# Performance work log

Hardware: AMD Instinct MI355X
Metric: run time of the kernel (lower is better)

Reference implementation:

```python
import jax, jax.numpy as jnp
import numpy as np

B, H, W, C = 1, 64, 64, 256
HEADS, K, DIL = 8, 7, 2
HD = C // HEADS
FF = 4 * C
EPS = 1e-5
SCALE = 1.0 / float(np.sqrt(HD))


def _axis_indices(L, k, d):
    """NATTEN dilated neighborhood: per dilation-group clamped sliding window.
    Returns key indices [L,k] and relative-position-bias indices [L,k]."""
    i = np.arange(L)
    g, rem = i // d, i % d                      # position within dilation group
    lg = (L - rem + d - 1) // d                 # group length per position
    start = np.clip(g - k // 2, 0, lg - k)      # clamped window start (group coords)
    a = np.arange(k)
    kidx = (start[:, None] + a[None, :]) * d + rem[:, None]          # key coord
    bidx = start[:, None] + a[None, :] - g[:, None] + (k - 1)        # rpb coord in [0, 2k-2]
    return kidx.astype(np.int32), bidx.astype(np.int32)


def setup_inputs():
    key = jax.random.key(0)
    ks = jax.random.split(key, 8)
    p = lambda k_, sh: jax.random.normal(k_, sh, jnp.float32) * 0.02
    return {
        "x": jax.random.normal(ks[0], (B, H, W, C), jnp.float32),
        "ln1_g": jnp.ones((C,), jnp.float32), "ln1_b": jnp.zeros((C,), jnp.float32),
        "wq": p(ks[1], (C, C)), "bq": jnp.zeros((C,), jnp.float32),
        "wk": p(ks[2], (C, C)), "bk": jnp.zeros((C,), jnp.float32),
        "wv": p(ks[3], (C, C)), "bv": jnp.zeros((C,), jnp.float32),
        "rpb": p(ks[4], (HEADS, 2 * K - 1, 2 * K - 1)),
        "wo": p(ks[5], (C, C)), "bo": jnp.zeros((C,), jnp.float32),
        "ln2_g": jnp.ones((C,), jnp.float32), "ln2_b": jnp.zeros((C,), jnp.float32),
        "w1": p(ks[6], (C, FF)), "b1": jnp.zeros((FF,), jnp.float32),
        "w2": p(ks[7], (FF, C)), "b2": jnp.zeros((C,), jnp.float32),
    }


def _layer_norm(x, g, b):
    m = jnp.mean(x, -1, keepdims=True)
    v = jnp.mean(jnp.square(x - m), -1, keepdims=True)
    return (x - m) * jax.lax.rsqrt(v + EPS) * g + b


def reference(x, ln1_g, ln1_b, wq, bq, wk, bk, wv, bv, rpb, wo, bo,
              ln2_g, ln2_b, w1, b1, w2, b2):
    ih, bih = _axis_indices(H, K, DIL)   # [H,K]
    iw, biw = _axis_indices(W, K, DIL)   # [W,K]
    hs = _layer_norm(x, ln1_g, ln1_b)
    q = (hs @ wq + bq).reshape(B, H, W, HEADS, HD) * SCALE
    k = (hs @ wk + bk).reshape(B, H, W, HEADS, HD)
    v = (hs @ wv + bv).reshape(B, H, W, HEADS, HD)
    # gather dilated neighborhoods -> [B,H,W,K,K,heads,hd]
    k_nb = k[:, ih[:, None, :, None], iw[None, :, None, :], :, :]
    v_nb = v[:, ih[:, None, :, None], iw[None, :, None, :], :, :]
    # natten2dqkrpb: per-query scores over K*K dilated neighbors + rpb
    scores = jnp.einsum('bijnc,bijklnc->bnijkl', q, k_nb)
    bias = rpb[:, bih[:, None, :, None], biw[None, :, None, :]]  # [heads,H,W,K,K]
    scores = scores + bias[None]
    probs = jax.nn.softmax(scores.reshape(B, HEADS, H, W, K * K), axis=-1)
    # natten2dav
    ctx = jnp.einsum('bnijp,bijpnc->bijnc', probs,
                     v_nb.reshape(B, H, W, K * K, HEADS, HD))
    attn_out = ctx.reshape(B, H, W, C) @ wo + bo
    hs2 = x + attn_out                      # residual (layer_scale disabled: init 0.0)
    y = _layer_norm(hs2, ln2_g, ln2_b)
    y = jax.nn.gelu(y @ w1 + b1, approximate=False) @ w2 + b2
    return hs2 + y
```

## Files before the change

kernel.cpp:

```cpp
#include <hip/hip_runtime.h>
#include <math.h>

#define CC 256
#define NTOK 4096
#define NHEADS 8
#define HD 32
#define FFD 1024
#define LN_EPS 1e-5f
#define QSCALE 0.17677669529663687f

typedef __bf16 bf16x8 __attribute__((ext_vector_type(8)));
typedef float f32x4 __attribute__((ext_vector_type(4)));
typedef unsigned short u16x8 __attribute__((ext_vector_type(8)));

__device__ __forceinline__ unsigned short f2bf(float f) {
    unsigned u = __builtin_bit_cast(unsigned, f);
    u += 0x7fff + ((u >> 16) & 1);
    return (unsigned short)(u >> 16);
}
__device__ __forceinline__ float bf2f(unsigned short h) {
    unsigned u = ((unsigned)h) << 16;
    return __builtin_bit_cast(float, u);
}
__device__ __forceinline__ void gload16(const unsigned short* g, unsigned short* l) {
    __builtin_amdgcn_global_load_lds(
        (const __attribute__((address_space(1))) unsigned int*)(const void*)g,
        (__attribute__((address_space(3))) unsigned int*)(void*)l, 16, 0, 0);
}

__device__ __forceinline__ void ln_row(const float* __restrict__ x, const float* __restrict__ g,
                                       const float* __restrict__ b, unsigned short* __restrict__ out,
                                       int tok, int lane) {
    const float4 v = ((const float4*)(x + (size_t)tok * CC))[lane];
    float s  = v.x + v.y + v.z + v.w;
    float ss = v.x * v.x + v.y * v.y + v.z * v.z + v.w * v.w;
    #pragma unroll
    for (int o = 32; o > 0; o >>= 1) { s += __shfl_xor(s, o); ss += __shfl_xor(ss, o); }
    float m   = s * (1.0f / CC);
    float var = ss * (1.0f / CC) - m * m;
    float r   = rsqrtf(var + LN_EPS);
    float4 gv = ((const float4*)g)[lane];
    float4 bv = ((const float4*)b)[lane];
    ushort4 o4;
    o4.x = f2bf((v.x - m) * r * gv.x + bv.x);
    o4.y = f2bf((v.y - m) * r * gv.y + bv.y);
    o4.z = f2bf((v.z - m) * r * gv.z + bv.z);
    o4.w = f2bf((v.w - m) * r * gv.w + bv.w);
    ((ushort4*)(out + (size_t)tok * CC))[lane] = o4;
}

__global__ void ln_kernel(const float* __restrict__ x, const float* __restrict__ g,
                          const float* __restrict__ b, unsigned short* __restrict__ out) {
    ln_row(x, g, b, out, blockIdx.x * 4 + (threadIdx.x >> 6), threadIdx.x & 63);
}

__global__ void setup_kernel(const float* __restrict__ wq, const float* __restrict__ wk,
                             const float* __restrict__ wv, const float* __restrict__ wo,
                             const float* __restrict__ w1, const float* __restrict__ w2,
                             const float* __restrict__ bq, const float* __restrict__ bk,
                             const float* __restrict__ bv,
                             const float* __restrict__ x, const float* __restrict__ ln1_g,
                             const float* __restrict__ ln1_b,
                             unsigned short* __restrict__ wt_qkv, unsigned short* __restrict__ wo_t,
                             unsigned short* __restrict__ w1_t, unsigned short* __restrict__ w2_t,
                             float* __restrict__ bqkv, unsigned short* __restrict__ hs_bf) {
    int id = blockIdx.x;
    int t = threadIdx.x;
    if (id >= 193) {
        ln_row(x, ln1_g, ln1_b, hs_bf, (id - 193) * 4 + (t >> 6), t & 63);
        return;
    }
    if (id == 192) {
        bqkv[t]       = bq[t] * QSCALE;
        bqkv[256 + t] = bk[t];
        bqkv[512 + t] = bv[t];
        return;
    }
    const float* src; unsigned short* dst;
    int Kd, N, rowoff = 0, bx, by; float scale = 1.0f;
    if (id < 16)       { src = wq; dst = wt_qkv; Kd = 256;  N = 256;  scale = QSCALE; int l = id;       bx = l & 3;  by = l >> 2; }
    else if (id < 32)  { src = wk; dst = wt_qkv; Kd = 256;  N = 256;  rowoff = 256;   int l = id - 16;  bx = l & 3;  by = l >> 2; }
    else if (id < 48)  { src = wv; dst = wt_qkv; Kd = 256;  N = 256;  rowoff = 512;   int l = id - 32;  bx = l & 3;  by = l >> 2; }
    else if (id < 64)  { src = wo; dst = wo_t;   Kd = 256;  N = 256;                  int l = id - 48;  bx = l & 3;  by = l >> 2; }
    else if (id < 128) { src = w1; dst = w1_t;   Kd = 256;  N = 1024;                 int l = id - 64;  bx = l & 15; by = l >> 4; }
    else               { src = w2; dst = w2_t;   Kd = 1024; N = 256;                  int l = id - 128; bx = l & 3;  by = l >> 2; }
    int n0 = bx * 64, k0 = by * 64;
    __shared__ float tile[64][65];
    int cc = t & 63, rb = t >> 6;
    #pragma unroll
    for (int i = 0; i < 16; i++) {
        int r = rb + i * 4;
        tile[r][cc] = src[(size_t)(k0 + r) * N + n0 + cc];
    }
    __syncthreads();
    int n = t >> 2;
    #pragma unroll
    for (int i = 0; i < 8; i++) {
        int p = (t & 3) + i * 4;
        unsigned lo = f2bf(tile[2 * p][n] * scale);
        unsigned hi = f2bf(tile[2 * p + 1][n] * scale);
        *(unsigned*)(dst + (size_t)(rowoff + n0 + n) * Kd + k0 + 2 * p) = lo | (hi << 16);
    }
}

template<int BM, int BN, int KD, int ACT, bool ADD_RES, bool OUT_BF16>
__global__ __launch_bounds__(256) void gemm_tb(
    const unsigned short* __restrict__ A, const unsigned short* __restrict__ Bt,
    const float* __restrict__ bias, const float* __restrict__ res,
    void* __restrict__ Cm, int N) {
    constexpr int WM = BM / 2, WN = BN / 2;
    constexpr int MF = WM / 16, NF = WN / 16;
    constexpr int NIT = KD / 64;
    constexpr int LA = BM * 8 / 256;
    constexpr int LB = BN * 8 / 256;
    constexpr int L  = LA + LB;
    __shared__ unsigned short lds[3][(BM + BN) * 64];
    const int t = threadIdx.x;
    const int lane = t & 63, w = t >> 6;
    const int wr = w >> 1, wc = w & 1;
    const int bm = blockIdx.y * BM, bn = blockIdx.x * BN;
    const int fr = lane & 15, sq = lane >> 4;

    auto stage = [&](int it, int buf) {
        unsigned short* La = lds[buf];
        unsigned short* Lb = lds[buf] + BM * 64;
        #pragma unroll
        for (int i = 0; i < LA; i++) {
            int c = t + i * 256;
            int kk = c / (BM * 4), r = (c % (BM * 4)) >> 2, jj = c & 3;
            gload16(A + (size_t)(bm + r) * KD + it * 64 + kk * 32 + jj * 8, La + c * 8);
        }
        #pragma unroll
        for (int i = 0; i < LB; i++) {
            int c = t + i * 256;
            int kk = c / (BN * 4), r = (c % (BN * 4)) >> 2, jj = c & 3;
            gload16(Bt + (size_t)(bn + r) * KD + it * 64 + kk * 32 + jj * 8, Lb + c * 8);
        }
    };

    f32x4 acc[MF][NF] = {};
    stage(0, 0);
    stage(1, 1);
    #pragma unroll
    for (int it = 0; it < NIT; ++it) {
        if (it < NIT - 1) {
            if constexpr (L == 4) asm volatile("s_waitcnt vmcnt(4)" ::: "memory");
            else if constexpr (L == 3) asm volatile("s_waitcnt vmcnt(3)" ::: "memory");
            else asm volatile("s_waitcnt vmcnt(2)" ::: "memory");
        } else {
            asm volatile("s_waitcnt vmcnt(0)" ::: "memory");
        }
        __builtin_amdgcn_s_barrier();
        if (it + 2 < NIT) stage(it + 2, (it + 2) % 3);
        const int buf = it % 3;
        #pragma unroll
        for (int kk = 0; kk < 2; kk++) {
            const char* La = (const char*)(lds[buf]) + kk * BM * 64;
            const char* Lb = (const char*)(lds[buf] + BM * 64) + kk * BN * 64;
            bf16x8 af[MF], bfr[NF];
            #pragma unroll
            for (int i = 0; i < MF; i++)
                af[i] = *(const bf16x8*)(La + (wr * WM + i * 16 + fr) * 64 + sq * 16);
            #pragma unroll
            for (int j = 0; j < NF; j++)
                bfr[j] = *(const bf16x8*)(Lb + (wc * WN + j * 16 + fr) * 64 + sq * 16);
            #pragma unroll
            for (int i = 0; i < MF; i++)
                #pragma unroll
                for (int j = 0; j < NF; j++)
                    acc[i][j] = __builtin_amdgcn_mfma_f32_16x16x32_bf16(af[i], bfr[j], acc[i][j], 0, 0, 0);
        }
    }
    #pragma unroll
    for (int i = 0; i < MF; i++) {
        int row0 = bm + wr * WM + i * 16 + sq * 4;
        #pragma unroll
        for (int j = 0; j < NF; j++) {
            int col = bn + wc * WN + j * 16 + fr;
            float bvv = bias[col];
            #pragma unroll
            for (int r = 0; r < 4; r++) {
                float v = acc[i][j][r] + bvv;
                if constexpr (ACT == 1) v = 0.5f * v * (1.0f + erff(v * 0.70710678118654752f));
                if constexpr (ADD_RES) v += res[(size_t)(row0 + r) * N + col];
                if constexpr (OUT_BF16)
                    ((unsigned short*)Cm)[(size_t)(row0 + r) * N + col] = f2bf(v);
                else
                    ((float*)Cm)[(size_t)(row0 + r) * N + col] = v;
            }
        }
    }
}

__global__ __launch_bounds__(256) void attn_mfma(
    const unsigned short* __restrict__ qkv, const float* __restrict__ rpb,
    unsigned short* __restrict__ ctx) {
    __shared__ __align__(16) unsigned short VT[128][136];
    __shared__ __align__(16) unsigned short Pl[4][16][136];
    __shared__ unsigned short tbl[16][112];
    __shared__ float rpbl[4][172];

    const int t = threadIdx.x;
    const int lane = t & 63, w = t >> 6;
    const int fr = lane & 15, sq = lane >> 4;
    const int bid = blockIdx.x;
    const int p = bid & 3, tile = (bid >> 2) & 63, hb = bid >> 8;
    const int ri = p >> 1, rj = p & 1;
    const int tgi = (tile >> 3) * 4, tgj = (tile & 7) * 4;
    const int kgi0 = min(max(tgi - 3, 0), 22);
    const int kgj0 = min(max(tgj - 3, 0), 22);
    const int head = hb * 4 + w;

    for (int i = lane; i < 169; i += 64)
        rpbl[w][i] = rpb[head * 169 + i];
    if (lane == 0) rpbl[w][169] = -1e30f;

    for (int e = t; e < 16 * 112; e += 256) {
        int q = e / 112, kk = e % 112;
        unsigned short idx = 169;
        if (kk < 100) {
            int kr = kk / 10, kc = kk % 10;
            int qgi = tgi + (q >> 2), qgj = tgj + (q & 3);
            int kgi = kgi0 + kr, kgj = kgj0 + kc;
            int si = min(max(qgi - 3, 0), 25), sj = min(max(qgj - 3, 0), 25);
            if (kgi >= si && kgi <= si + 6 && kgj >= sj && kgj <= sj + 6)
                idx = (unsigned short)((kgi - qgi + 6) * 13 + (kgj - qgj + 6));
        }
        tbl[q][kk] = idx;
    }

    for (int c0 = t; c0 < 1600; c0 += 256) {
        int key = c0 >> 4, ch8 = c0 & 15;
        int kr = key / 10, kc = key % 10;
        int kt = ((kgi0 + kr) * 2 + ri) * 64 + (kgj0 + kc) * 2 + rj;
        u16x8 vv = *(const u16x8*)(qkv + (size_t)kt * 768 + 512 + hb * 128 + ch8 * 8);
        #pragma unroll
        for (int e = 0; e < 8; e++) VT[ch8 * 8 + e][key] = vv[e];
    }
    for (int c0 = t; c0 < 128 * 14; c0 += 256) {
        int row = c0 / 14, cp = c0 % 14;
        *(unsigned*)&VT[row][100 + cp * 2] = 0;
    }
    __syncthreads();

    const int qtok = ((tgi + (fr >> 2)) * 2 + ri) * 64 + (tgj + (fr & 3)) * 2 + rj;
    bf16x8 qf = *(const bf16x8*)(qkv + (size_t)qtok * 768 + head * 32 + sq * 8);

    f32x4 sc[7];
    __builtin_amdgcn_s_setprio(1);
    #pragma unroll
    for (int c = 0; c < 7; c++) {
        int kk = c * 16 + fr;
        if (kk > 99) kk = 99;
        int kr = kk / 10, kc = kk % 10;
        int kt = ((kgi0 + kr) * 2 + ri) * 64 + (kgj0 + kc) * 2 + rj;
        bf16x8 kf = *(const bf16x8*)(qkv + (size_t)kt * 768 + 256 + head * 32 + sq * 8);
        f32x4 z = {0.0f, 0.0f, 0.0f, 0.0f};
        sc[c] = __builtin_amdgcn_mfma_f32_16x16x32_bf16(kf, qf, z, 0, 0, 0);
    }
    __builtin_amdgcn_s_setprio(0);
    #pragma unroll
    for (int c = 0; c < 7; c++)
        #pragma unroll
        for (int r = 0; r < 4; r++) {
            int idx = tbl[fr][c * 16 + 4 * sq + r];
            sc[c][r] += rpbl[w][idx];
        }

    float mx = -1e30f;
    #pragma unroll
    for (int c = 0; c < 7; c++)
        #pragma unroll
        for (int r = 0; r < 4; r++) mx = fmaxf(mx, sc[c][r]);
    mx = fmaxf(mx, __shfl_xor(mx, 16));
    mx = fmaxf(mx, __shfl_xor(mx, 32));
    float sum = 0.0f;
    #pragma unroll
    for (int c = 0; c < 7; c++)
        #pragma unroll
        for (int r = 0; r < 4; r++) {
            sc[c][r] = __expf(sc[c][r] - mx);
            sum += sc[c][r];
        }
    sum += __shfl_xor(sum, 16);
    sum += __shfl_xor(sum, 32);
    float inv = 1.0f / sum;

    #pragma unroll
    for (int c = 0; c < 7; c++)
        #pragma unroll
        for (int r = 0; r < 4; r++)
            Pl[w][fr][c * 16 + 4 * sq + r] = f2bf(sc[c][r] * inv);
    *(unsigned long long*)&Pl[w][fr][112 + sq * 4] = 0ull;

    f32x4 o0 = {0, 0, 0, 0}, o1 = {0, 0, 0, 0};
    __builtin_amdgcn_s_setprio(1);
    #pragma unroll
    for (int m = 0; m < 4; m++) {
        bf16x8 pf = *(const bf16x8*)(&Pl[w][fr][m * 32 + sq * 8]);
        bf16x8 v0 = *(const bf16x8*)(&VT[w * 32 + fr][m * 32 + sq * 8]);
        bf16x8 v1 = *(const bf16x8*)(&VT[w * 32 + 16 + fr][m * 32 + sq * 8]);
        o0 = __builtin_amdgcn_mfma_f32_16x16x32_bf16(pf, v0, o0, 0, 0, 0);
        o1 = __builtin_amdgcn_mfma_f32_16x16x32_bf16(pf, v1, o1, 0, 0, 0);
    }
    __builtin_amdgcn_s_setprio(0);
    #pragma unroll
    for (int r = 0; r < 4; r++) {
        int tok = ((tgi + sq) * 2 + ri) * 64 + (tgj + r) * 2 + rj;
        ctx[(size_t)tok * 256 + head * 32 + fr]      = f2bf(o0[r]);
        ctx[(size_t)tok * 256 + head * 32 + 16 + fr] = f2bf(o1[r]);
    }
}

extern "C" void kernel_launch(void* const* d_in, const int* in_sizes, int n_in,
                              void* d_out, int out_size, void* d_ws, size_t ws_size,
                              hipStream_t stream) {
    const float* x     = (const float*)d_in[0];
    const float* ln1_g = (const float*)d_in[1];
    const float* ln1_b = (const float*)d_in[2];
    const float* wq    = (const float*)d_in[3];
    const float* bq    = (const float*)d_in[4];
    const float* wk    = (const float*)d_in[5];
    const float* bk    = (const float*)d_in[6];
    const float* wv    = (const float*)d_in[7];
    const float* bv    = (const float*)d_in[8];
    const float* rpb   = (const float*)d_in[9];
    const float* wo    = (const float*)d_in[10];
    const float* bo    = (const float*)d_in[11];
    const float* ln2_g = (const float*)d_in[12];
    const float* ln2_b = (const float*)d_in[13];
    const float* w1    = (const float*)d_in[14];
    const float* b1    = (const float*)d_in[15];
    const float* w2    = (const float*)d_in[16];
    const float* b2    = (const float*)d_in[17];

    char* wsb = (char*)d_ws;
    unsigned short* hs_bf  = (unsigned short*)(wsb);
    unsigned short* qkv_bf = (unsigned short*)(wsb + (2u << 20));
    unsigned short* ctx_bf = (unsigned short*)(wsb + (8u << 20));
    float*          hs2    = (float*)(wsb + (10u << 20));
    unsigned short* y1_bf  = (unsigned short*)(wsb + (14u << 20));
    unsigned short* gm_bf  = (unsigned short*)(wsb + (16u << 20));
    unsigned short* wt_qkv = (unsigned short*)(wsb + (24u << 20));
    unsigned short* wo_t   = wt_qkv + 768 * 256;
    unsigned short* w1_t   = wo_t + 256 * 256;
    unsigned short* w2_t   = w1_t + 1024 * 256;
    float*          bqkv   = (float*)(w2_t + 256 * 1024);

    setup_kernel<<<1217, 256, 0, stream>>>(wq, wk, wv, wo, w1, w2, bq, bk, bv,
                                           x, ln1_g, ln1_b,
                                           wt_qkv, wo_t, w1_t, w2_t, bqkv, hs_bf);
    gemm_tb<64, 64, 256, 0, false, true><<<dim3(12, 64), 256, 0, stream>>>(
        hs_bf, wt_qkv, bqkv, nullptr, qkv_bf, 768);
    attn_mfma<<<512, 256, 0, stream>>>(qkv_bf, rpb, ctx_bf);
    gemm_tb<32, 64, 256, 0, true, false><<<dim3(4, 128), 256, 0, stream>>>(
        ctx_bf, wo_t, bo, x, hs2, 256);
    ln_kernel<<<NTOK / 4, 256, 0, stream>>>(hs2, ln2_g, ln2_b, y1_bf);
    gemm_tb<64, 64, 256, 1, false, true><<<dim3(16, 64), 256, 0, stream>>>(
        y1_bf, w1_t, b1, nullptr, gm_bf, 1024);
    gemm_tb<32, 64, 1024, 0, true, false><<<dim3(4, 128), 256, 0, stream>>>(
        gm_bf, w2_t, b2, hs2, (float*)d_out, 256);
}
```

Baseline: 133.8 us.

## Fuse all stages into one persistent kernel with atomic grid barriers

Replaces seven separate kernel launches with a single persistent kernel of 256 blocks. Each block loops over its share of tiles for every stage, and stages are separated by a software grid barrier built on an atomic counter and sleep polling. The aim is to remove launch overhead and inter-kernel gaps. In exchange, 256 blocks may underfill the GPU for the GEMM and attention stages, the spin barrier adds its own cost, and correctness depends on all blocks being co-resident.

Result: slower. 246.1 us (+83.9%).

```diff
diff --git a/kernel.cpp b/kernel.cpp
--- a/kernel.cpp
+++ b/kernel.cpp
@@ -3,11 +3,9 @@
 
 #define CC 256
 #define NTOK 4096
-#define NHEADS 8
-#define HD 32
-#define FFD 1024
 #define LN_EPS 1e-5f
 #define QSCALE 0.17677669529663687f
+#define NBLK 256
 
 typedef __bf16 bf16x8 __attribute__((ext_vector_type(8)));
 typedef float f32x4 __attribute__((ext_vector_type(4)));
@@ -26,6 +24,18 @@
     __builtin_amdgcn_global_load_lds(
         (const __attribute__((address_space(1))) unsigned int*)(const void*)g,
         (__attribute__((address_space(3))) unsigned int*)(void*)l, 16, 0, 0);
+}
+
+__device__ __forceinline__ void grid_sync(unsigned* bar) {
+    __syncthreads();
+    if (threadIdx.x == 0) {
+        __threadfence();
+        unsigned old = atomicAdd(bar, 1u);
+        unsigned target = (old / NBLK + 1u) * NBLK;
+        while (atomicAdd(bar, 0u) < target) __builtin_amdgcn_s_sleep(8);
+        __threadfence();
+    }
+    __syncthreads();
 }
 
 __device__ __forceinline__ void ln_row(const float* __restrict__ x, const float* __restrict__ g,
@@ -49,81 +59,27 @@
     ((ushort4*)(out + (size_t)tok * CC))[lane] = o4;
 }
 
-__global__ void ln_kernel(const float* __restrict__ x, const float* __restrict__ g,
-                          const float* __restrict__ b, unsigned short* __restrict__ out) {
-    ln_row(x, g, b, out, blockIdx.x * 4 + (threadIdx.x >> 6), threadIdx.x & 63);
-}
-
-__global__ void setup_kernel(const float* __restrict__ wq, const float* __restrict__ wk,
-                             const float* __restrict__ wv, const float* __restrict__ wo,
-                             const float* __restrict__ w1, const float* __restrict__ w2,
-                             const float* __restrict__ bq, const float* __restrict__ bk,
-                             const float* __restrict__ bv,
-                             const float* __restrict__ x, const float* __restrict__ ln1_g,
-                             const float* __restrict__ ln1_b,
-                             unsigned short* __restrict__ wt_qkv, unsigned short* __restrict__ wo_t,
-                             unsigned short* __restrict__ w1_t, unsigned short* __restrict__ w2_t,
-                             float* __restrict__ bqkv, unsigned short* __restrict__ hs_bf) {
-    int id = blockIdx.x;
-    int t = threadIdx.x;
-    if (id >= 193) {
-        ln_row(x, ln1_g, ln1_b, hs_bf, (id - 193) * 4 + (t >> 6), t & 63);
-        return;
-    }
-    if (id == 192) {
-        bqkv[t]       = bq[t] * QSCALE;
-        bqkv[256 + t] = bk[t];
-        bqkv[512 + t] = bv[t];
-        return;
-    }
-    const float* src; unsigned short* dst;
-    int Kd, N, rowoff = 0, bx, by; float scale = 1.0f;
-    if (id < 16)       { src = wq; dst = wt_qkv; Kd = 256;  N = 256;  scale = QSCALE; int l = id;       bx = l & 3;  by = l >> 2; }
-    else if (id < 32)  { src = wk; dst = wt_qkv; Kd = 256;  N = 256;  rowoff = 256;   int l = id - 16;  bx = l & 3;  by = l >> 2; }
-    else if (id < 48)  { src = wv; dst = wt_qkv; Kd = 256;  N = 256;  rowoff = 512;   int l = id - 32;  bx = l & 3;  by = l >> 2; }
-    else if (id < 64)  { src = wo; dst = wo_t;   Kd = 256;  N = 256;                  int l = id - 48;  bx = l & 3;  by = l >> 2; }
-    else if (id < 128) { src = w1; dst = w1_t;   Kd = 256;  N = 1024;                 int l = id - 64;  bx = l & 15; by = l >> 4; }
-    else               { src = w2; dst = w2_t;   Kd = 1024; N = 256;                  int l = id - 128; bx = l & 3;  by = l >> 2; }
-    int n0 = bx * 64, k0 = by * 64;
-    __shared__ float tile[64][65];
-    int cc = t & 63, rb = t >> 6;
-    #pragma unroll
-    for (int i = 0; i < 16; i++) {
-        int r = rb + i * 4;
-        tile[r][cc] = src[(size_t)(k0 + r) * N + n0 + cc];
-    }
-    __syncthreads();
-    int n = t >> 2;
-    #pragma unroll
-    for (int i = 0; i < 8; i++) {
-        int p = (t & 3) + i * 4;
-        unsigned lo = f2bf(tile[2 * p][n] * scale);
-        unsigned hi = f2bf(tile[2 * p + 1][n] * scale);
-        *(unsigned*)(dst + (size_t)(rowoff + n0 + n) * Kd + k0 + 2 * p) = lo | (hi << 16);
-    }
-}
-
 template<int BM, int BN, int KD, int ACT, bool ADD_RES, bool OUT_BF16>
-__global__ __launch_bounds__(256) void gemm_tb(
-    const unsigned short* __restrict__ A, const unsigned short* __restrict__ Bt,
-    const float* __restrict__ bias, const float* __restrict__ res,
-    void* __restrict__ Cm, int N) {
+__device__ void gemm_tile(char* smem, const unsigned short* __restrict__ A,
+                          const unsigned short* __restrict__ Bt,
+                          const float* __restrict__ bias, const float* __restrict__ res,
+                          void* __restrict__ Cm, int N, int bm, int bn) {
     constexpr int WM = BM / 2, WN = BN / 2;
     constexpr int MF = WM / 16, NF = WN / 16;
     constexpr int NIT = KD / 64;
     constexpr int LA = BM * 8 / 256;
     constexpr int LB = BN * 8 / 256;
     constexpr int L  = LA + LB;
-    __shared__ unsigned short lds[3][(BM + BN) * 64];
+    constexpr int BUFE = (BM + BN) * 64;
+    unsigned short* lds = (unsigned short*)smem;
     const int t = threadIdx.x;
     const int lane = t & 63, w = t >> 6;
     const int wr = w >> 1, wc = w & 1;
-    const int bm = blockIdx.y * BM, bn = blockIdx.x * BN;
     const int fr = lane & 15, sq = lane >> 4;
 
     auto stage = [&](int it, int buf) {
-        unsigned short* La = lds[buf];
-        unsigned short* Lb = lds[buf] + BM * 64;
+        unsigned short* La = lds + buf * BUFE;
+        unsigned short* Lb = La + BM * 64;
         #pragma unroll
         for (int i = 0; i < LA; i++) {
             int c = t + i * 256;
@@ -141,22 +97,20 @@
     f32x4 acc[MF][NF] = {};
     stage(0, 0);
     stage(1, 1);
-    #pragma unroll
     for (int it = 0; it < NIT; ++it) {
         if (it < NIT - 1) {
             if constexpr (L == 4) asm volatile("s_waitcnt vmcnt(4)" ::: "memory");
-            else if constexpr (L == 3) asm volatile("s_waitcnt vmcnt(3)" ::: "memory");
-            else asm volatile("s_waitcnt vmcnt(2)" ::: "memory");
+            else asm volatile("s_waitcnt vmcnt(3)" ::: "memory");
         } else {
             asm volatile("s_waitcnt vmcnt(0)" ::: "memory");
         }
         __builtin_amdgcn_s_barrier();
         if (it + 2 < NIT) stage(it + 2, (it + 2) % 3);
-        const int buf = it % 3;
+        const char* Lab = (const char*)(lds + (it % 3) * BUFE);
         #pragma unroll
         for (int kk = 0; kk < 2; kk++) {
-            const char* La = (const char*)(lds[buf]) + kk * BM * 64;
-            const char* Lb = (const char*)(lds[buf] + BM * 64) + kk * BN * 64;
+            const char* La = Lab + kk * BM * 64;
+            const char* Lb = Lab + BM * 128 + kk * BN * 64;
             bf16x8 af[MF], bfr[NF];
             #pragma unroll
             for (int i = 0; i < MF; i++)
@@ -190,30 +144,33 @@
             }
         }
     }
-}
-
-__global__ __launch_bounds__(256) void attn_mfma(
-    const unsigned short* __restrict__ qkv, const float* __restrict__ rpb,
-    unsigned short* __restrict__ ctx) {
-    __shared__ __align__(16) unsigned short VT[128][136];
-    __shared__ __align__(16) unsigned short Pl[4][16][136];
-    __shared__ unsigned short tbl[16][112];
-    __shared__ float rpbl[4][172];
+    asm volatile("s_waitcnt vmcnt(0)" ::: "memory");
+    __syncthreads();
+}
+
+__device__ void attn_unit(char* smem, const unsigned short* __restrict__ qkv,
+                          const float* __restrict__ rpb, unsigned short* __restrict__ ctx,
+                          int unit) {
+    unsigned short* VT  = (unsigned short*)smem;
+    unsigned short* Pl  = VT + 128 * 136;
+    unsigned short* tbl = Pl + 4 * 16 * 136;
+    float*          rpbl = (float*)(tbl + 16 * 112);
 
     const int t = threadIdx.x;
     const int lane = t & 63, w = t >> 6;
     const int fr = lane & 15, sq = lane >> 4;
-    const int bid = blockIdx.x;
-    const int p = bid & 3, tile = (bid >> 2) & 63, hb = bid >> 8;
+    const int p = unit & 3, tile = (unit >> 2) & 63, hb = unit >> 8;
     const int ri = p >> 1, rj = p & 1;
     const int tgi = (tile >> 3) * 4, tgj = (tile & 7) * 4;
     const int kgi0 = min(max(tgi - 3, 0), 22);
     const int kgj0 = min(max(tgj - 3, 0), 22);
     const int head = hb * 4 + w;
 
+    __syncthreads();
+
     for (int i = lane; i < 169; i += 64)
-        rpbl[w][i] = rpb[head * 169 + i];
-    if (lane == 0) rpbl[w][169] = -1e30f;
+        rpbl[w * 172 + i] = rpb[head * 169 + i];
+    if (lane == 0) rpbl[w * 172 + 169] = -1e30f;
 
     for (int e = t; e < 16 * 112; e += 256) {
         int q = e / 112, kk = e % 112;
@@ -226,7 +183,7 @@
             if (kgi >= si && kgi <= si + 6 && kgj >= sj && kgj <= sj + 6)
                 idx = (unsigned short)((kgi - qgi + 6) * 13 + (kgj - qgj + 6));
         }
-        tbl[q][kk] = idx;
+        tbl[q * 112 + kk] = idx;
     }
 
     for (int c0 = t; c0 < 1600; c0 += 256) {
@@ -235,11 +192,11 @@
         int kt = ((kgi0 + kr) * 2 + ri) * 64 + (kgj0 + kc) * 2 + rj;
         u16x8 vv = *(const u16x8*)(qkv + (size_t)kt * 768 + 512 + hb * 128 + ch8 * 8);
         #pragma unroll
-        for (int e = 0; e < 8; e++) VT[ch8 * 8 + e][key] = vv[e];
+        for (int e = 0; e < 8; e++) VT[(ch8 * 8 + e) * 136 + key] = vv[e];
     }
     for (int c0 = t; c0 < 128 * 14; c0 += 256) {
         int row = c0 / 14, cp = c0 % 14;
-        *(unsigned*)&VT[row][100 + cp * 2] = 0;
+        *(unsigned*)&VT[row * 136 + 100 + cp * 2] = 0;
     }
     __syncthreads();
 
@@ -262,10 +219,8 @@
     #pragma unroll
     for (int c = 0; c < 7; c++)
         #pragma unroll
-        for (int r = 0; r < 4; r++) {
-            int idx = tbl[fr][c * 16 + 4 * sq + r];
-            sc[c][r] += rpbl[w][idx];
-        }
+        for (int r = 0; r < 4; r++)
+            sc[c][r] += rpbl[w * 172 + tbl[fr * 112 + c * 16 + 4 * sq + r]];
 
     float mx = -1e30f;
     #pragma unroll
@@ -290,16 +245,16 @@
     for (int c = 0; c < 7; c++)
         #pragma unroll
         for (int r = 0; r < 4; r++)
-            Pl[w][fr][c * 16 + 4 * sq + r] = f2bf(sc[c][r] * inv);
-    *(unsigned long long*)&Pl[w][fr][112 + sq * 4] = 0ull;
+            Pl[(w * 16 + fr) * 136 + c * 16 + 4 * sq + r] = f2bf(sc[c][r] * inv);
+    *(unsigned long long*)&Pl[(w * 16 + fr) * 136 + 112 + sq * 4] = 0ull;
 
     f32x4 o0 = {0, 0, 0, 0}, o1 = {0, 0, 0, 0};
     __builtin_amdgcn_s_setprio(1);
     #pragma unroll
     for (int m = 0; m < 4; m++) {
-        bf16x8 pf = *(const bf16x8*)(&Pl[w][fr][m * 32 + sq * 8]);
-        bf16x8 v0 = *(const bf16x8*)(&VT[w * 32 + fr][m * 32 + sq * 8]);
-        bf16x8 v1 = *(const bf16x8*)(&VT[w * 32 + 16 + fr][m * 32 + sq * 8]);
+        bf16x8 pf = *(const bf16x8*)(&Pl[(w * 16 + fr) * 136 + m * 32 + sq * 8]);
+        bf16x8 v0 = *(const bf16x8*)(&VT[(w * 32 + fr) * 136 + m * 32 + sq * 8]);
+        bf16x8 v1 = *(const bf16x8*)(&VT[(w * 32 + 16 + fr) * 136 + m * 32 + sq * 8]);
         o0 = __builtin_amdgcn_mfma_f32_16x16x32_bf16(pf, v0, o0, 0, 0, 0);
         o1 = __builtin_amdgcn_mfma_f32_16x16x32_bf16(pf, v1, o1, 0, 0, 0);
     }
@@ -309,6 +264,104 @@
         int tok = ((tgi + sq) * 2 + ri) * 64 + (tgj + r) * 2 + rj;
         ctx[(size_t)tok * 256 + head * 32 + fr]      = f2bf(o0[r]);
         ctx[(size_t)tok * 256 + head * 32 + 16 + fr] = f2bf(o1[r]);
+    }
+}
+
+__global__ __launch_bounds__(256) void mega(
+    const float* __restrict__ x,
+    const float* __restrict__ ln1_g, const float* __restrict__ ln1_b,
+    const float* __restrict__ wq, const float* __restrict__ bq,
+    const float* __restrict__ wk, const float* __restrict__ bk,
+    const float* __restrict__ wv, const float* __restrict__ bv,
+    const float* __restrict__ rpb,
+    const float* __restrict__ wo, const float* __restrict__ bo,
+    const float* __restrict__ ln2_g, const float* __restrict__ ln2_b,
+    const float* __restrict__ w1, const float* __restrict__ b1,
+    const float* __restrict__ w2, const float* __restrict__ b2,
+    unsigned short* __restrict__ hs_bf, unsigned short* __restrict__ qkv_bf,
+    unsigned short* __restrict__ ctx_bf, float* __restrict__ hs2,
+    unsigned short* __restrict__ y1_bf, unsigned short* __restrict__ gm_bf,
+    unsigned short* __restrict__ wt_qkv, unsigned short* __restrict__ wo_t,
+    unsigned short* __restrict__ w1_t, unsigned short* __restrict__ w2_t,
+    float* __restrict__ bqkv, float* __restrict__ out, unsigned* bar) {
+    __shared__ __align__(16) char smem[58560];
+    const int b = blockIdx.x;
+    const int t = threadIdx.x;
+
+    if (b < 192) {
+        const float* src; unsigned short* dst;
+        int Kd, N, rowoff = 0, bx, by; float scale = 1.0f;
+        if (b < 16)       { src = wq; dst = wt_qkv; Kd = 256;  N = 256;  scale = QSCALE; int l = b;       bx = l & 3;  by = l >> 2; }
+        else if (b < 32)  { src = wk; dst = wt_qkv; Kd = 256;  N = 256;  rowoff = 256;   int l = b - 16;  bx = l & 3;  by = l >> 2; }
+        else if (b < 48)  { src = wv; dst = wt_qkv; Kd = 256;  N = 256;  rowoff = 512;   int l = b - 32;  bx = l & 3;  by = l >> 2; }
+        else if (b < 64)  { src = wo; dst = wo_t;   Kd = 256;  N = 256;                  int l = b - 48;  bx = l & 3;  by = l >> 2; }
+        else if (b < 128) { src = w1; dst = w1_t;   Kd = 256;  N = 1024;                 int l = b - 64;  bx = l & 15; by = l >> 4; }
+        else              { src = w2; dst = w2_t;   Kd = 1024; N = 256;                  int l = b - 128; bx = l & 3;  by = l >> 2; }
+        int n0 = bx * 64, k0 = by * 64;
+        float (*tile)[65] = (float(*)[65])smem;
+        int cc = t & 63, rb = t >> 6;
+        #pragma unroll
+        for (int i = 0; i < 16; i++) {
+            int r = rb + i * 4;
+            tile[r][cc] = src[(size_t)(k0 + r) * N + n0 + cc];
+        }
+        __syncthreads();
+        int n = t >> 2;
+        #pragma unroll
+        for (int i = 0; i < 8; i++) {
+            int pp = (t & 3) + i * 4;
+            unsigned lo = f2bf(tile[2 * pp][n] * scale);
+            unsigned hi = f2bf(tile[2 * pp + 1][n] * scale);
+            *(unsigned*)(dst + (size_t)(rowoff + n0 + n) * Kd + k0 + 2 * pp) = lo | (hi << 16);
+        }
+    } else if (b == 192) {
+        bqkv[t]       = bq[t] * QSCALE;
+        bqkv[256 + t] = bk[t];
+        bqkv[512 + t] = bv[t];
+    }
+    #pragma unroll
+    for (int k2 = 0; k2 < 4; k2++) {
+        int q = b * 4 + k2;
+        ln_row(x, ln1_g, ln1_b, hs_bf, q * 4 + (t >> 6), t & 63);
+    }
+    grid_sync(bar);
+
+    for (int k2 = 0; k2 < 3; k2++) {
+        int tid = b * 3 + k2;
+        gemm_tile<64, 64, 256, 0, false, true>(smem, hs_bf, wt_qkv, bqkv, nullptr,
+                                               qkv_bf, 768, (tid / 12) * 64, (tid % 12) * 64);
+    }
+    grid_sync(bar);
+
+    for (int k2 = 0; k2 < 2; k2++)
+        attn_unit(smem, qkv_bf, rpb, ctx_bf, b * 2 + k2);
+    grid_sync(bar);
+
+    for (int k2 = 0; k2 < 2; k2++) {
+        int tid = b * 2 + k2;
+        gemm_tile<32, 64, 256, 0, true, false>(smem, ctx_bf, wo_t, bo, x,
+                                               hs2, 256, (tid / 4) * 32, (tid % 4) * 64);
+    }
+    grid_sync(bar);
+
+    #pragma unroll
+    for (int k2 = 0; k2 < 4; k2++) {
+        int q = b * 4 + k2;
+        ln_row(hs2, ln2_g, ln2_b, y1_bf, q * 4 + (t >> 6), t & 63);
+    }
+    grid_sync(bar);
+
+    for (int k2 = 0; k2 < 4; k2++) {
+        int tid = b * 4 + k2;
+        gemm_tile<64, 64, 256, 1, false, true>(smem, y1_bf, w1_t, b1, nullptr,
+                                               gm_bf, 1024, (tid / 16) * 64, (tid % 16) * 64);
+    }
+    grid_sync(bar);
+
+    for (int k2 = 0; k2 < 2; k2++) {
+        int tid = b * 2 + k2;
+        gemm_tile<32, 64, 1024, 0, true, false>(smem, gm_bf, w2_t, b2, hs2,
+                                                out, 256, (tid / 4) * 32, (tid % 4) * 64);
     }
 }
 
@@ -346,18 +399,12 @@
     unsigned short* w1_t   = wo_t + 256 * 256;
     unsigned short* w2_t   = w1_t + 1024 * 256;
     float*          bqkv   = (float*)(w2_t + 256 * 1024);
-
-    setup_kernel<<<1217, 256, 0, stream>>>(wq, wk, wv, wo, w1, w2, bq, bk, bv,
-                                           x, ln1_g, ln1_b,
-                                           wt_qkv, wo_t, w1_t, w2_t, bqkv, hs_bf);
-    gemm_tb<64, 64, 256, 0, false, true><<<dim3(12, 64), 256, 0, stream>>>(
-        hs_bf, wt_qkv, bqkv, nullptr, qkv_bf, 768);
-    attn_mfma<<<512, 256, 0, stream>>>(qkv_bf, rpb, ctx_bf);
-    gemm_tb<32, 64, 256, 0, true, false><<<dim3(4, 128), 256, 0, stream>>>(
-        ctx_bf, wo_t, bo, x, hs2, 256);
-    ln_kernel<<<NTOK / 4, 256, 0, stream>>>(hs2, ln2_g, ln2_b, y1_bf);
-    gemm_tb<64, 64, 256, 1, false, true><<<dim3(16, 64), 256, 0, stream>>>(
-        y1_bf, w1_t, b1, nullptr, gm_bf, 1024);
-    gemm_tb<32, 64, 1024, 0, true, false><<<dim3(4, 128), 256, 0, stream>>>(
-        gm_bf, w2_t, b2, hs2, (float*)d_out, 256);
-}
+    unsigned*       bar    = (unsigned*)(wsb + (40u << 20));
+
+    hipMemsetAsync(bar, 0, 64, stream);
+    mega<<<NBLK, 256, 0, stream>>>(x, ln1_g, ln1_b, wq, bq, wk, bk, wv, bv, rpb,
+                                   wo, bo, ln2_g, ln2_b, w1, b1, w2, b2,
+                                   hs_bf, qkv_bf, ctx_bf, hs2, y1_bf, gm_bf,
+                                   wt_qkv, wo_t, w1_t, w2_t, bqkv,
+                                   (float*)d_out, bar);
+}
```
